# Optimization experiments

Measured on AMD Instinct MI355X. Metric: run time of the kernel, lower is better.

The kernel has to match this reference:

```python
import jax, jax.numpy as jnp
import numpy as np

RADIUS = 0.1
NSAMPLE = 32


def _ball_query(radius, nsample, xyz, new_xyz):
    # xyz: (B,N,3), new_xyz: (B,npoint,3) -> idx (B,npoint,nsample) int32
    # Faithful to the CUDA ball_query: take the first nsample in-radius indices
    # (in ascending point order); pad with the first found index.
    N = xyz.shape[1]
    d2 = jnp.sum((new_xyz[:, :, None, :] - xyz[:, None, :, :]) ** 2, axis=-1)  # (B,np,N)
    mask = d2 < radius * radius
    key_arr = jnp.where(mask, jnp.arange(N, dtype=jnp.int32), jnp.int32(N))
    idx = jnp.sort(key_arr, axis=-1)[..., :nsample]  # (B,np,ns)
    first = idx[..., :1]
    idx = jnp.where(idx == N, first, idx)
    idx = jnp.where(idx == N, 0, idx)  # empty-ball fallback (matches zero-init buffer)
    return idx


def _group(features, idx):
    # features (B,C,N), idx (B,np,ns) -> (B,C,np,ns)
    return jax.vmap(lambda f, i: f[:, i])(features, idx)


def _forward(xyz, new_xyz):
    idx = jax.lax.stop_gradient(_ball_query(RADIUS, NSAMPLE, xyz, new_xyz))
    xyz_t = jnp.transpose(xyz, (0, 2, 1))                 # (B,3,N)
    g = _group(xyz_t, idx)                                # (B,3,np,ns) grouped_xyz
    c = jnp.transpose(new_xyz, (0, 2, 1))[..., None]      # (B,3,np,1)  new_xyz_reshaped

    # pairwise distances within each group
    diff = g[..., :, None] - g[..., None, :]              # (B,3,np,ns,ns)
    dis = jnp.sqrt(jnp.sum(diff * diff, axis=1))          # (B,np,ns,ns)
    mean_dis = jnp.mean(dis, axis=3)                      # (B,np,ns)
    tip_idx = jnp.argmax(mean_dis, axis=2)                # (B,np)
    tip_pts = jnp.take_along_axis(g, tip_idx[:, None, :, None], axis=3)[..., 0]  # (B,3,np)

    cb = jnp.broadcast_to(c, g.shape)                     # (B,3,np,ns)
    gpv = jnp.cross(jnp.cross(cb, g, axis=1), cb, axis=1)
    gpv = gpv / jnp.linalg.norm(gpv, axis=1)[:, None]     # (B,3,np,ns)

    new_r = jnp.sqrt(jnp.sum(c * c, axis=1))              # (B,np,1)
    new_norm = c / (new_r[:, None] + 1e-8)                # (B,3,np,1)

    c3 = c[..., 0]                                        # (B,3,np)
    tpv = jnp.cross(jnp.cross(c3, tip_pts, axis=1), c3, axis=1)
    tpv = tpv / jnp.linalg.norm(tpv, axis=1)[:, None]     # (B,3,np)

    gcv = jnp.cross(gpv, jnp.broadcast_to(tpv[..., None], gpv.shape), axis=1)
    sinv = jnp.sum(gcv * new_norm, axis=1)                # (B,np,ns)

    dis_t = jnp.transpose(dis, (0, 2, 1, 3))              # (B,ns,np,ns)
    dis_sort = jnp.sort(dis_t, axis=1) * sinv[:, None]    # (B,ns,np,ns)
    grouped_r = jnp.sqrt(jnp.sum(g * g, axis=1))          # (B,np,ns)
    return jnp.concatenate([dis_sort, grouped_r[:, None]], axis=1)  # (B,ns+1,np,ns)


def setup_inputs() -> dict:
    key = jax.random.key(0)
    k1, k2 = jax.random.split(key)
    xyz = jax.random.uniform(k1, (4, 16384, 3), dtype=jnp.float32)
    new_xyz = jax.random.uniform(k2, (4, 2048, 3), dtype=jnp.float32)
    return {"xyz": xyz, "new_xyz": new_xyz}


def reference(xyz, new_xyz):
    return _forward(xyz, new_xyz)
```

## Files before the change

### kernel.cpp

```cpp
#include <hip/hip_runtime.h>


#define BB 4
#define NN 16384
#define MM 2048
#define NS 32
#define R2 0.01f
#define NCELL 1000
#define CPAD 1024
#define HCAP 128

#define WS_PTS_OFF (16 * 1024)
#define WS_NEED (WS_PTS_OFF + (size_t)BB * NN * 16)

__device__ __forceinline__ int cell_of(float x, float y, float z) {
    int ci = (int)(x * 10.0f); ci = ci < 0 ? 0 : (ci > 9 ? 9 : ci);
    int cj = (int)(y * 10.0f); cj = cj < 0 ? 0 : (cj > 9 ? 9 : cj);
    int ck = (int)(z * 10.0f); ck = ck < 0 ? 0 : (ck > 9 ? 9 : ck);
    return (ci * 10 + cj) * 10 + ck;
}

__global__ __launch_bounds__(1024) void k_build(const float* __restrict__ xyz,
                                                int* __restrict__ off,
                                                float4* __restrict__ pts) {
    __shared__ int sc[1024];
    __shared__ int sa[1024];
    const int b = blockIdx.x, t = threadIdx.x;
    sc[t] = 0;
    __syncthreads();
    const float* xp = xyz + (size_t)b * NN * 3;
    float X[16], Y[16], Z[16]; int C[16];
    #pragma unroll
    for (int k = 0; k < 16; ++k) {
        int i = k * 1024 + t;
        const float* p = xp + (size_t)i * 3;
        X[k] = p[0]; Y[k] = p[1]; Z[k] = p[2];
        C[k] = cell_of(X[k], Y[k], Z[k]);
        atomicAdd(&sc[C[k]], 1);
    }
    __syncthreads();
    int v = sc[t];
    sa[t] = v;
    __syncthreads();
    for (int s = 1; s < 1024; s <<= 1) {
        int u = (t >= s) ? sa[t - s] : 0;
        __syncthreads();
        sa[t] += u;
        __syncthreads();
    }
    int excl = sa[t] - v;
    if (t < NCELL) off[b * CPAD + t] = excl;
    if (t == NCELL - 1) off[b * CPAD + NCELL] = sa[t];
    __syncthreads();
    sc[t] = excl;
    __syncthreads();
    #pragma unroll
    for (int k = 0; k < 16; ++k) {
        int pos = atomicAdd(&sc[C[k]], 1);
        int i = k * 1024 + t;
        pts[(size_t)b * NN + pos] = make_float4(X[k], Y[k], Z[k], __int_as_float(i));
    }
}

__global__ __launch_bounds__(256) void qgr_grid_kernel(
    const float* __restrict__ xyz,
    const float* __restrict__ nxyz,
    const int* __restrict__ offi,
    const float4* __restrict__ pts,
    float* __restrict__ out) {

    __shared__ float s_hx[4][HCAP], s_hy[4][HCAP], s_hz[4][HCAP];
    __shared__ int   s_hidx[4][HCAP];

    const int lane = threadIdx.x & 63;
    const int w = threadIdx.x >> 6;
    const int q = blockIdx.x * 4 + w;
    const int b = q >> 11;
    const int m = q & (MM - 1);

    const float* xb = xyz + (size_t)b * NN * 3;
    const float* nq = nxyz + (size_t)q * 3;
    const float cx = nq[0], cy = nq[1], cz = nq[2];
    const unsigned long long lmask = (1ull << lane) - 1ull;

    const int* offb = offi + b * CPAD;
    const float4* ptsb = pts + (size_t)b * NN;

    int ci0 = (int)(cx * 10.0f); ci0 = ci0 < 0 ? 0 : (ci0 > 9 ? 9 : ci0);
    int cj0 = (int)(cy * 10.0f); cj0 = cj0 < 0 ? 0 : (cj0 > 9 ? 9 : cj0);
    int ck0 = (int)(cz * 10.0f); ck0 = ck0 < 0 ? 0 : (ck0 > 9 ? 9 : ck0);
    int zlo = ck0 > 0 ? ck0 - 1 : 0;
    int zhi = ck0 < 9 ? ck0 + 1 : 9;

    int rs[9], rl[9];
    #pragma unroll
    for (int r = 0; r < 9; ++r) { rs[r] = 0; rl[r] = 0; }
    int nr = 0;
    #pragma unroll
    for (int di = -1; di <= 1; ++di) {
        int ii = ci0 + di; if ((unsigned)ii > 9u) continue;
        #pragma unroll
        for (int dj = -1; dj <= 1; ++dj) {
            int jj = cj0 + dj; if ((unsigned)jj > 9u) continue;
            int base2 = (ii * 10 + jj) * 10;
            int s0 = offb[base2 + zlo];
            int e0 = offb[base2 + zhi + 1];
            int len = e0 - s0;
            if (len > 0) { rs[nr] = s0; rl[nr] = len; ++nr; }
        }
    }

    float4 P[9];
    #pragma unroll
    for (int r = 0; r < 9; ++r) {
        int a = (lane < rl[r]) ? (rs[r] + lane) : 0;
        P[r] = ptsb[a];
    }

    int hits = 0;
    #pragma unroll
    for (int r = 0; r < 9; ++r) {
        float dx = __fsub_rn(cx, P[r].x);
        float dy = __fsub_rn(cy, P[r].y);
        float dz = __fsub_rn(cz, P[r].z);
        float d2 = __fadd_rn(__fadd_rn(__fmul_rn(dx, dx), __fmul_rn(dy, dy)),
                             __fmul_rn(dz, dz));
        bool hit = (lane < rl[r]) && (d2 < R2);
        unsigned long long bal = __ballot(hit);
        if (bal) {
            int rank = __popcll(bal & lmask);
            int slot = hits + rank;
            if (hit && slot < HCAP) {
                s_hx[w][slot] = P[r].x; s_hy[w][slot] = P[r].y;
                s_hz[w][slot] = P[r].z; s_hidx[w][slot] = __float_as_int(P[r].w);
            }
            hits += __popcll(bal);
        }
    }
    for (int r = 0; r < nr; ++r) {
        for (int t0 = 64; t0 < rl[r]; t0 += 64) {
            int t = t0 + lane;
            bool act = t < rl[r];
            float4 Q = ptsb[rs[r] + (act ? t : 0)];
            float dx = __fsub_rn(cx, Q.x);
            float dy = __fsub_rn(cy, Q.y);
            float dz = __fsub_rn(cz, Q.z);
            float d2 = __fadd_rn(__fadd_rn(__fmul_rn(dx, dx), __fmul_rn(dy, dy)),
                                 __fmul_rn(dz, dz));
            bool hit = act && (d2 < R2);
            unsigned long long bal = __ballot(hit);
            if (bal) {
                int rank = __popcll(bal & lmask);
                int slot = hits + rank;
                if (hit && slot < HCAP) {
                    s_hx[w][slot] = Q.x; s_hy[w][slot] = Q.y;
                    s_hz[w][slot] = Q.z; s_hidx[w][slot] = __float_as_int(Q.w);
                }
                hits += __popcll(bal);
            }
        }
    }

    int cap = hits < HCAP ? hits : HCAP;
    int key0 = (lane < cap)      ? ((s_hidx[w][lane] << 8) | lane)            : 0x7fffffff;
    int key1 = (64 + lane < cap) ? ((s_hidx[w][64 + lane] << 8) | (64 + lane)) : 0x7fffffff;

    #pragma unroll
    for (int k = 2; k <= 128; k <<= 1) {
        #pragma unroll
        for (int j = k >> 1; j > 0; j >>= 1) {
            if (j >= 64) {
                int lo = min(key0, key1), hi = max(key0, key1);
                key0 = lo; key1 = hi;
            } else {
                int p0 = __shfl_xor(key0, j);
                int p1 = __shfl_xor(key1, j);
                bool lower = (lane & j) == 0;
                bool up0, up1;
                if (k >= 128)     { up0 = true;             up1 = true; }
                else if (k == 64) { up0 = true;             up1 = false; }
                else              { up0 = (lane & k) == 0;  up1 = up0; }
                key0 = (lower == up0) ? min(key0, p0) : max(key0, p0);
                key1 = (lower == up1) ? min(key1, p1) : max(key1, p1);
            }
        }
    }

    const int found = hits < NS ? hits : NS;
    const int j = lane & 31;
    int skey = __shfl(key0, j);
    float hx = 0.f, hy = 0.f, hz = 0.f;
    if (j < found) {
        int s = skey & 0xFF;
        hx = s_hx[w][s]; hy = s_hy[w][s]; hz = s_hz[w][s];
    }
    float p0x, p0y, p0z;
    if (found == 0) { p0x = xb[0]; p0y = xb[1]; p0z = xb[2]; }
    else { p0x = __shfl(hx, 0); p0y = __shfl(hy, 0); p0z = __shfl(hz, 0); }
    if (j >= found) { hx = p0x; hy = p0y; hz = p0z; }

    float v[NS];
    #pragma unroll
    for (int ii = 0; ii < NS; ++ii) {
        float bx = __shfl(hx, ii), by = __shfl(hy, ii), bz = __shfl(hz, ii);
        float dx = __fsub_rn(bx, hx);
        float dy = __fsub_rn(by, hy);
        float dz = __fsub_rn(bz, hz);
        v[ii] = sqrtf(__fadd_rn(__fadd_rn(__fmul_rn(dx, dx), __fmul_rn(dy, dy)),
                                __fmul_rn(dz, dz)));
    }

    float r8[8];
    #pragma unroll
    for (int t = 0; t < 8; ++t) {
        r8[t] = __fadd_rn(__fadd_rn(__fadd_rn(v[t], v[t + 8]), v[t + 16]), v[t + 24]);
    }
    float mv = __fadd_rn(__fadd_rn(__fadd_rn(r8[0], r8[1]), __fadd_rn(r8[2], r8[3])),
                         __fadd_rn(__fadd_rn(r8[4], r8[5]), __fadd_rn(r8[6], r8[7])));
    int mi = j;
    #pragma unroll
    for (int off = 1; off < 64; off <<= 1) {
        float ov = __shfl_xor(mv, off);
        int oi = __shfl_xor(mi, off);
        if (ov > mv || (ov == mv && oi < mi)) { mv = ov; mi = oi; }
    }

    float tx = __shfl(hx, mi), ty = __shfl(hy, mi), tz = __shfl(hz, mi);

    float ux = cy * tz - cz * ty, uy = cz * tx - cx * tz, uz = cx * ty - cy * tx;
    float vx = uy * cz - uz * cy, vy = uz * cx - ux * cz, vz = ux * cy - uy * cx;
    float vn = fmaxf(sqrtf(vx * vx + vy * vy + vz * vz), 1e-37f);
    float tnx = vx / vn, tny = vy / vn, tnz = vz / vn;

    float nrm = sqrtf(cx * cx + cy * cy + cz * cz);
    float dn = nrm + 1e-8f;
    float nnx = cx / dn, nny = cy / dn, nnz = cz / dn;

    float ax = cy * hz - cz * hy, ay = cz * hx - cx * hz, az = cx * hy - cy * hx;
    float px = ay * cz - az * cy, py = az * cx - ax * cz, pz = ax * cy - ay * cx;
    float pn = fmaxf(sqrtf(px * px + py * py + pz * pz), 1e-37f);
    px /= pn; py /= pn; pz /= pn;

    float qx = py * tnz - pz * tny;
    float qy = pz * tnx - px * tnz;
    float qz = px * tny - py * tnx;
    float sinv = qx * nnx + qy * nny + qz * nnz;

    float gr = sqrtf(hx * hx + hy * hy + hz * hz);

    const size_t rowstride = (size_t)MM * NS;
    const size_t obase = (((size_t)b * 33) * MM + m) * NS + j;
    if (lane < NS) out[obase + 32 * rowstride] = gr;

    #pragma unroll
    for (int k = 2; k <= NS; k <<= 1) {
        #pragma unroll
        for (int jj = k >> 1; jj > 0; jj >>= 1) {
            #pragma unroll
            for (int ii = 0; ii < NS; ++ii) {
                int ll = ii ^ jj;
                if (ll > ii) {
                    bool up = ((ii & k) == 0);
                    float a = v[ii], c2 = v[ll];
                    bool sw = up ? (a > c2) : (a < c2);
                    if (sw) { v[ii] = c2; v[ll] = a; }
                }
            }
        }
    }

    if (lane < NS) {
        #pragma unroll
        for (int ii = 0; ii < NS; ++ii)
            out[obase + (size_t)ii * rowstride] = v[ii] * sinv;
    }
}

#define CHUNKS 4
__global__ __launch_bounds__(256) void qgr_kernel(
    const float* __restrict__ xyz,
    const float* __restrict__ nxyz,
    float* __restrict__ out) {

    __shared__ float s_gx[4][NS], s_gy[4][NS], s_gz[4][NS];
    __shared__ float s_dis[4][NS][NS + 1];

    const int lane = threadIdx.x & 63;
    const int w = threadIdx.x >> 6;
    const int q = blockIdx.x * 4 + w;
    const int b = q >> 11;
    const int m = q & (MM - 1);

    const float* xb = xyz + (size_t)b * NN * 3;
    const float* nq = nxyz + (size_t)q * 3;
    const float cx = nq[0], cy = nq[1], cz = nq[2];
    const unsigned long long lmask = (1ull << lane) - 1ull;

    int cnt = 0;
    for (int base = 0; base < NN; base += 64 * CHUNKS) {
        float X[CHUNKS], Y[CHUNKS], Z[CHUNKS];
        #pragma unroll
        for (int c = 0; c < CHUNKS; ++c) {
            const float* p = xb + (size_t)(base + c * 64 + lane) * 3;
            X[c] = p[0]; Y[c] = p[1]; Z[c] = p[2];
        }
        bool in[CHUNKS];
        #pragma unroll
        for (int c = 0; c < CHUNKS; ++c) {
            float dx = __fsub_rn(cx, X[c]);
            float dy = __fsub_rn(cy, Y[c]);
            float dz = __fsub_rn(cz, Z[c]);
            float d2 = __fadd_rn(__fadd_rn(__fmul_rn(dx, dx), __fmul_rn(dy, dy)),
                                 __fmul_rn(dz, dz));
            in[c] = d2 < R2;
        }
        #pragma unroll
        for (int c = 0; c < CHUNKS; ++c) {
            unsigned long long bal = __ballot(in[c]);
            if (bal) {
                int rank = __popcll(bal & lmask);
                int slot = cnt + rank;
                if (in[c] && slot < NS) {
                    s_gx[w][slot] = X[c]; s_gy[w][slot] = Y[c]; s_gz[w][slot] = Z[c];
                }
                cnt += __popcll(bal);
            }
        }
        if (cnt >= NS) break;
    }
    __syncthreads();

    int found = cnt < NS ? cnt : NS;
    float p0x, p0y, p0z;
    if (found == 0) { p0x = xb[0]; p0y = xb[1]; p0z = xb[2]; }
    else            { p0x = s_gx[w][0]; p0y = s_gy[w][0]; p0z = s_gz[w][0]; }
    if (lane < NS && lane >= found) {
        s_gx[w][lane] = p0x; s_gy[w][lane] = p0y; s_gz[w][lane] = p0z;
    }
    __syncthreads();

    #pragma unroll
    for (int t = 0; t < 16; ++t) {
        int e = t * 64 + lane;
        int di = e >> 5, dj = e & 31;
        float dx = __fsub_rn(s_gx[w][di], s_gx[w][dj]);
        float dy = __fsub_rn(s_gy[w][di], s_gy[w][dj]);
        float dz = __fsub_rn(s_gz[w][di], s_gz[w][dj]);
        s_dis[w][di][dj] =
            sqrtf(__fadd_rn(__fadd_rn(__fmul_rn(dx, dx), __fmul_rn(dy, dy)), __fmul_rn(dz, dz)));
    }
    __syncthreads();

    {
        int i = lane & 31;
        float r[8];
        #pragma unroll
        for (int t = 0; t < 8; ++t) {
            r[t] = __fadd_rn(__fadd_rn(__fadd_rn(s_dis[w][i][t], s_dis[w][i][t + 8]),
                                        s_dis[w][i][t + 16]),
                             s_dis[w][i][t + 24]);
        }
        float mv = __fadd_rn(__fadd_rn(__fadd_rn(r[0], r[1]), __fadd_rn(r[2], r[3])),
                             __fadd_rn(__fadd_rn(r[4], r[5]), __fadd_rn(r[6], r[7])));
        int mi = i;
        #pragma unroll
        for (int off = 1; off < 64; off <<= 1) {
            float ov = __shfl_xor(mv, off);
            int oi = __shfl_xor(mi, off);
            if (ov > mv || (ov == mv && oi < mi)) { mv = ov; mi = oi; }
        }
        float tx = s_gx[w][mi], ty = s_gy[w][mi], tz = s_gz[w][mi];
        float ux = cy * tz - cz * ty, uy = cz * tx - cx * tz, uz = cx * ty - cy * tx;
        float vx = uy * cz - uz * cy, vy = uz * cx - ux * cz, vz = ux * cy - uy * cx;
        float vn = fmaxf(sqrtf(vx * vx + vy * vy + vz * vz), 1e-37f);
        float tnx = vx / vn, tny = vy / vn, tnz = vz / vn;
        float nr = sqrtf(cx * cx + cy * cy + cz * cz);
        float dn = nr + 1e-8f;
        float nnx = cx / dn, nny = cy / dn, nnz = cz / dn;
        int j = lane & 31;
        float gx = s_gx[w][j], gy = s_gy[w][j], gz = s_gz[w][j];
        float ax = cy * gz - cz * gy, ay = cz * gx - cx * gz, az = cx * gy - cy * gx;
        float px = ay * cz - az * cy, py = az * cx - ax * cz, pz = ax * cy - ay * cx;
        float pn = fmaxf(sqrtf(px * px + py * py + pz * pz), 1e-37f);
        px /= pn; py /= pn; pz /= pn;
        float qx = py * tnz - pz * tny;
        float qy = pz * tnx - px * tnz;
        float qz = px * tny - py * tnx;
        float sinv = qx * nnx + qy * nny + qz * nnz;
        float gr = sqrtf(gx * gx + gy * gy + gz * gz);
        const size_t rowstride = (size_t)MM * NS;
        const size_t obase = (((size_t)b * 33) * MM + m) * NS + j;
        if (lane < NS) out[obase + 32 * rowstride] = gr;
        float v[NS];
        #pragma unroll
        for (int ii = 0; ii < NS; ++ii) v[ii] = s_dis[w][ii][j];
        #pragma unroll
        for (int k = 2; k <= NS; k <<= 1) {
            #pragma unroll
            for (int jj = k >> 1; jj > 0; jj >>= 1) {
                #pragma unroll
                for (int ii = 0; ii < NS; ++ii) {
                    int ll = ii ^ jj;
                    if (ll > ii) {
                        bool up = ((ii & k) == 0);
                        float a = v[ii], c2 = v[ll];
                        bool sw = up ? (a > c2) : (a < c2);
                        if (sw) { v[ii] = c2; v[ll] = a; }
                    }
                }
            }
        }
        if (lane < NS) {
            #pragma unroll
            for (int ii = 0; ii < NS; ++ii)
                out[obase + (size_t)ii * rowstride] = v[ii] * sinv;
        }
    }
}

extern "C" void kernel_launch(void* const* d_in, const int* in_sizes, int n_in,
                              void* d_out, int out_size, void* d_ws, size_t ws_size,
                              hipStream_t stream) {
    (void)in_sizes; (void)n_in; (void)out_size;
    const float* xyz = (const float*)d_in[0];
    const float* nxyz = (const float*)d_in[1];
    float* out = (float*)d_out;

    if (d_ws != nullptr && ws_size >= WS_NEED) {
        char* ws = (char*)d_ws;
        int* off = (int*)ws;
        float4* pts = (float4*)(ws + WS_PTS_OFF);
        k_build<<<BB, 1024, 0, stream>>>(xyz, off, pts);
        qgr_grid_kernel<<<(BB * MM) / 4, 256, 0, stream>>>(xyz, nxyz, off, pts, out);
    } else {
        qgr_kernel<<<(BB * MM) / 4, 256, 0, stream>>>(xyz, nxyz, out);
    }
}
```

Baseline: 114.8 us.

## Process two queries per wavefront and use shuffle-based scan in grid build

The grid query kernel now has each 64-lane wavefront handle two query points. The neighbor search runs sequentially for both, and each 32-lane half then runs the sort, pairwise-distance and output stages for its own query, so all lanes do useful work in the per-group compute instead of half idling. The hit-index sort becomes a 32-lane bitonic sort over four registers per lane. The build kernel replaces the shared-memory Hillis-Steele prefix scan, which needed many barriers, with a wave shuffle scan plus per-wave sums. In exchange, the two neighbor searches run back to back, which lengthens that phase per wave, and the launch uses half as many blocks.

New measurement: 105.3 us. 8.2% less time.

```diff
diff --git a/kernel.cpp b/kernel.cpp
--- a/kernel.cpp
+++ b/kernel.cpp
@@ -24,8 +24,9 @@
                                                 int* __restrict__ off,
                                                 float4* __restrict__ pts) {
     __shared__ int sc[1024];
-    __shared__ int sa[1024];
+    __shared__ int wsum[16];
     const int b = blockIdx.x, t = threadIdx.x;
+    const int lane = t & 63, wid = t >> 6;
     sc[t] = 0;
     __syncthreads();
     const float* xp = xyz + (size_t)b * NN * 3;
@@ -40,17 +41,21 @@
     }
     __syncthreads();
     int v = sc[t];
-    sa[t] = v;
-    __syncthreads();
-    for (int s = 1; s < 1024; s <<= 1) {
-        int u = (t >= s) ? sa[t - s] : 0;
-        __syncthreads();
-        sa[t] += u;
-        __syncthreads();
-    }
-    int excl = sa[t] - v;
+    int x = v;
+    #pragma unroll
+    for (int o = 1; o < 64; o <<= 1) {
+        int u = __shfl_up(x, o);
+        if (lane >= o) x += u;
+    }
+    if (lane == 63) wsum[wid] = x;
+    __syncthreads();
+    int pre = 0;
+    #pragma unroll
+    for (int i2 = 0; i2 < 16; ++i2) pre += (i2 < wid) ? wsum[i2] : 0;
+    int incl = x + pre;
+    int excl = incl - v;
     if (t < NCELL) off[b * CPAD + t] = excl;
-    if (t == NCELL - 1) off[b * CPAD + NCELL] = sa[t];
+    if (t == 1023) off[b * CPAD + NCELL] = incl;
     __syncthreads();
     sc[t] = excl;
     __syncthreads();
@@ -69,140 +74,193 @@
     const float4* __restrict__ pts,
     float* __restrict__ out) {
 
-    __shared__ float s_hx[4][HCAP], s_hy[4][HCAP], s_hz[4][HCAP];
-    __shared__ int   s_hidx[4][HCAP];
+    __shared__ float s_hx[4][2][HCAP], s_hy[4][2][HCAP], s_hz[4][2][HCAP];
+    __shared__ int   s_hidx[4][2][HCAP];
 
     const int lane = threadIdx.x & 63;
     const int w = threadIdx.x >> 6;
-    const int q = blockIdx.x * 4 + w;
-    const int b = q >> 11;
-    const int m = q & (MM - 1);
+    const int sub = lane & 31;
+    const int half = lane >> 5;
+    const int q0 = blockIdx.x * 8 + w * 2;
+    const int b = q0 >> 11;
 
     const float* xb = xyz + (size_t)b * NN * 3;
-    const float* nq = nxyz + (size_t)q * 3;
-    const float cx = nq[0], cy = nq[1], cz = nq[2];
+    const float* nq = nxyz + (size_t)q0 * 3;
+    const float cx0 = nq[0], cy0 = nq[1], cz0 = nq[2];
+    const float cx1 = nq[3], cy1 = nq[4], cz1 = nq[5];
     const unsigned long long lmask = (1ull << lane) - 1ull;
 
     const int* offb = offi + b * CPAD;
     const float4* ptsb = pts + (size_t)b * NN;
 
-    int ci0 = (int)(cx * 10.0f); ci0 = ci0 < 0 ? 0 : (ci0 > 9 ? 9 : ci0);
-    int cj0 = (int)(cy * 10.0f); cj0 = cj0 < 0 ? 0 : (cj0 > 9 ? 9 : cj0);
-    int ck0 = (int)(cz * 10.0f); ck0 = ck0 < 0 ? 0 : (ck0 > 9 ? 9 : ck0);
-    int zlo = ck0 > 0 ? ck0 - 1 : 0;
-    int zhi = ck0 < 9 ? ck0 + 1 : 9;
-
-    int rs[9], rl[9];
-    #pragma unroll
-    for (int r = 0; r < 9; ++r) { rs[r] = 0; rl[r] = 0; }
-    int nr = 0;
-    #pragma unroll
-    for (int di = -1; di <= 1; ++di) {
-        int ii = ci0 + di; if ((unsigned)ii > 9u) continue;
-        #pragma unroll
-        for (int dj = -1; dj <= 1; ++dj) {
-            int jj = cj0 + dj; if ((unsigned)jj > 9u) continue;
-            int base2 = (ii * 10 + jj) * 10;
-            int s0 = offb[base2 + zlo];
-            int e0 = offb[base2 + zhi + 1];
-            int len = e0 - s0;
-            if (len > 0) { rs[nr] = s0; rl[nr] = len; ++nr; }
-        }
-    }
-
-    float4 P[9];
-    #pragma unroll
-    for (int r = 0; r < 9; ++r) {
-        int a = (lane < rl[r]) ? (rs[r] + lane) : 0;
-        P[r] = ptsb[a];
-    }
-
-    int hits = 0;
-    #pragma unroll
-    for (int r = 0; r < 9; ++r) {
-        float dx = __fsub_rn(cx, P[r].x);
-        float dy = __fsub_rn(cy, P[r].y);
-        float dz = __fsub_rn(cz, P[r].z);
-        float d2 = __fadd_rn(__fadd_rn(__fmul_rn(dx, dx), __fmul_rn(dy, dy)),
-                             __fmul_rn(dz, dz));
-        bool hit = (lane < rl[r]) && (d2 < R2);
-        unsigned long long bal = __ballot(hit);
-        if (bal) {
-            int rank = __popcll(bal & lmask);
-            int slot = hits + rank;
-            if (hit && slot < HCAP) {
-                s_hx[w][slot] = P[r].x; s_hy[w][slot] = P[r].y;
-                s_hz[w][slot] = P[r].z; s_hidx[w][slot] = __float_as_int(P[r].w);
-            }
-            hits += __popcll(bal);
-        }
-    }
-    for (int r = 0; r < nr; ++r) {
-        for (int t0 = 64; t0 < rl[r]; t0 += 64) {
-            int t = t0 + lane;
-            bool act = t < rl[r];
-            float4 Q = ptsb[rs[r] + (act ? t : 0)];
-            float dx = __fsub_rn(cx, Q.x);
-            float dy = __fsub_rn(cy, Q.y);
-            float dz = __fsub_rn(cz, Q.z);
+    int hits01[2];
+    for (int tq = 0; tq < 2; ++tq) {
+        const float ccx = tq ? cx1 : cx0;
+        const float ccy = tq ? cy1 : cy0;
+        const float ccz = tq ? cz1 : cz0;
+
+        int ci0 = (int)(ccx * 10.0f); ci0 = ci0 < 0 ? 0 : (ci0 > 9 ? 9 : ci0);
+        int cj0 = (int)(ccy * 10.0f); cj0 = cj0 < 0 ? 0 : (cj0 > 9 ? 9 : cj0);
+        int ck0 = (int)(ccz * 10.0f); ck0 = ck0 < 0 ? 0 : (ck0 > 9 ? 9 : ck0);
+        int zlo = ck0 > 0 ? ck0 - 1 : 0;
+        int zhi = ck0 < 9 ? ck0 + 1 : 9;
+
+        int rs[9], rl[9];
+        #pragma unroll
+        for (int r = 0; r < 9; ++r) { rs[r] = 0; rl[r] = 0; }
+        int nr = 0;
+        #pragma unroll
+        for (int di = -1; di <= 1; ++di) {
+            int ii = ci0 + di; if ((unsigned)ii > 9u) continue;
+            #pragma unroll
+            for (int dj = -1; dj <= 1; ++dj) {
+                int jj = cj0 + dj; if ((unsigned)jj > 9u) continue;
+                int base2 = (ii * 10 + jj) * 10;
+                int s0 = offb[base2 + zlo];
+                int e0 = offb[base2 + zhi + 1];
+                int len = e0 - s0;
+                if (len > 0) { rs[nr] = s0; rl[nr] = len; ++nr; }
+            }
+        }
+
+        float4 P[9];
+        #pragma unroll
+        for (int r = 0; r < 9; ++r) {
+            int a = (lane < rl[r]) ? (rs[r] + lane) : 0;
+            P[r] = ptsb[a];
+        }
+
+        int hits = 0;
+        #pragma unroll
+        for (int r = 0; r < 9; ++r) {
+            float dx = __fsub_rn(ccx, P[r].x);
+            float dy = __fsub_rn(ccy, P[r].y);
+            float dz = __fsub_rn(ccz, P[r].z);
             float d2 = __fadd_rn(__fadd_rn(__fmul_rn(dx, dx), __fmul_rn(dy, dy)),
                                  __fmul_rn(dz, dz));
-            bool hit = act && (d2 < R2);
+            bool hit = (lane < rl[r]) && (d2 < R2);
             unsigned long long bal = __ballot(hit);
             if (bal) {
                 int rank = __popcll(bal & lmask);
                 int slot = hits + rank;
                 if (hit && slot < HCAP) {
-                    s_hx[w][slot] = Q.x; s_hy[w][slot] = Q.y;
-                    s_hz[w][slot] = Q.z; s_hidx[w][slot] = __float_as_int(Q.w);
+                    s_hx[w][tq][slot] = P[r].x; s_hy[w][tq][slot] = P[r].y;
+                    s_hz[w][tq][slot] = P[r].z; s_hidx[w][tq][slot] = __float_as_int(P[r].w);
                 }
                 hits += __popcll(bal);
             }
         }
-    }
-
-    int cap = hits < HCAP ? hits : HCAP;
-    int key0 = (lane < cap)      ? ((s_hidx[w][lane] << 8) | lane)            : 0x7fffffff;
-    int key1 = (64 + lane < cap) ? ((s_hidx[w][64 + lane] << 8) | (64 + lane)) : 0x7fffffff;
-
-    #pragma unroll
-    for (int k = 2; k <= 128; k <<= 1) {
+        for (int r = 0; r < nr; ++r) {
+            for (int t0 = 64; t0 < rl[r]; t0 += 64) {
+                int t = t0 + lane;
+                bool act = t < rl[r];
+                float4 Q = ptsb[rs[r] + (act ? t : 0)];
+                float dx = __fsub_rn(ccx, Q.x);
+                float dy = __fsub_rn(ccy, Q.y);
+                float dz = __fsub_rn(ccz, Q.z);
+                float d2 = __fadd_rn(__fadd_rn(__fmul_rn(dx, dx), __fmul_rn(dy, dy)),
+                                     __fmul_rn(dz, dz));
+                bool hit = act && (d2 < R2);
+                unsigned long long bal = __ballot(hit);
+                if (bal) {
+                    int rank = __popcll(bal & lmask);
+                    int slot = hits + rank;
+                    if (hit && slot < HCAP) {
+                        s_hx[w][tq][slot] = Q.x; s_hy[w][tq][slot] = Q.y;
+                        s_hz[w][tq][slot] = Q.z; s_hidx[w][tq][slot] = __float_as_int(Q.w);
+                    }
+                    hits += __popcll(bal);
+                }
+            }
+        }
+        hits01[tq] = hits;
+    }
+
+    const int hits = half ? hits01[1] : hits01[0];
+    const int cap = hits < HCAP ? hits : HCAP;
+    const float ccx = half ? cx1 : cx0;
+    const float ccy = half ? cy1 : cy0;
+    const float ccz = half ? cz1 : cz0;
+
+    int key[4];
+    #pragma unroll
+    for (int r = 0; r < 4; ++r) {
+        int e = r * 32 + sub;
+        key[r] = (e < cap) ? ((s_hidx[w][half][e] << 8) | e) : 0x7fffffff;
+    }
+
+    #pragma unroll
+    for (int k = 2; k <= 16; k <<= 1) {
         #pragma unroll
         for (int j = k >> 1; j > 0; j >>= 1) {
-            if (j >= 64) {
-                int lo = min(key0, key1), hi = max(key0, key1);
-                key0 = lo; key1 = hi;
-            } else {
-                int p0 = __shfl_xor(key0, j);
-                int p1 = __shfl_xor(key1, j);
-                bool lower = (lane & j) == 0;
-                bool up0, up1;
-                if (k >= 128)     { up0 = true;             up1 = true; }
-                else if (k == 64) { up0 = true;             up1 = false; }
-                else              { up0 = (lane & k) == 0;  up1 = up0; }
-                key0 = (lower == up0) ? min(key0, p0) : max(key0, p0);
-                key1 = (lower == up1) ? min(key1, p1) : max(key1, p1);
-            }
+            bool lower = (sub & j) == 0;
+            bool asc = (sub & k) == 0;
+            bool keepmin = (lower == asc);
+            #pragma unroll
+            for (int r = 0; r < 4; ++r) {
+                int p = __shfl_xor(key[r], j);
+                key[r] = keepmin ? min(key[r], p) : max(key[r], p);
+            }
+        }
+    }
+    #pragma unroll
+    for (int j = 16; j > 0; j >>= 1) {
+        bool lower = (sub & j) == 0;
+        #pragma unroll
+        for (int r = 0; r < 4; ++r) {
+            int p = __shfl_xor(key[r], j);
+            bool asc = (r & 1) == 0;
+            key[r] = (lower == asc) ? min(key[r], p) : max(key[r], p);
+        }
+    }
+    {
+        int t0 = min(key[0], key[1]); key[1] = max(key[0], key[1]); key[0] = t0;
+        int t2 = max(key[2], key[3]); key[3] = min(key[2], key[3]); key[2] = t2;
+    }
+    #pragma unroll
+    for (int j = 16; j > 0; j >>= 1) {
+        bool lower = (sub & j) == 0;
+        #pragma unroll
+        for (int r = 0; r < 4; ++r) {
+            int p = __shfl_xor(key[r], j);
+            bool asc = (r & 2) == 0;
+            key[r] = (lower == asc) ? min(key[r], p) : max(key[r], p);
+        }
+    }
+    {
+        int t0 = min(key[0], key[2]); key[2] = max(key[0], key[2]); key[0] = t0;
+        int t1 = min(key[1], key[3]); key[3] = max(key[1], key[3]); key[1] = t1;
+        t0 = min(key[0], key[1]); key[1] = max(key[0], key[1]); key[0] = t0;
+        t1 = min(key[2], key[3]); key[3] = max(key[2], key[3]); key[2] = t1;
+    }
+    #pragma unroll
+    for (int j = 16; j > 0; j >>= 1) {
+        bool lower = (sub & j) == 0;
+        #pragma unroll
+        for (int r = 0; r < 4; ++r) {
+            int p = __shfl_xor(key[r], j);
+            key[r] = lower ? min(key[r], p) : max(key[r], p);
         }
     }
 
     const int found = hits < NS ? hits : NS;
-    const int j = lane & 31;
-    int skey = __shfl(key0, j);
+    const int hbase = half << 5;
     float hx = 0.f, hy = 0.f, hz = 0.f;
-    if (j < found) {
-        int s = skey & 0xFF;
-        hx = s_hx[w][s]; hy = s_hy[w][s]; hz = s_hz[w][s];
+    if (sub < found) {
+        int s = key[0] & 0xFF;
+        hx = s_hx[w][half][s]; hy = s_hy[w][half][s]; hz = s_hz[w][half][s];
     }
     float p0x, p0y, p0z;
     if (found == 0) { p0x = xb[0]; p0y = xb[1]; p0z = xb[2]; }
-    else { p0x = __shfl(hx, 0); p0y = __shfl(hy, 0); p0z = __shfl(hz, 0); }
-    if (j >= found) { hx = p0x; hy = p0y; hz = p0z; }
+    else { p0x = __shfl(hx, hbase); p0y = __shfl(hy, hbase); p0z = __shfl(hz, hbase); }
+    if (sub >= found) { hx = p0x; hy = p0y; hz = p0z; }
 
     float v[NS];
     #pragma unroll
     for (int ii = 0; ii < NS; ++ii) {
-        float bx = __shfl(hx, ii), by = __shfl(hy, ii), bz = __shfl(hz, ii);
+        float bx = __shfl(hx, hbase + ii);
+        float by = __shfl(hy, hbase + ii);
+        float bz = __shfl(hz, hbase + ii);
         float dx = __fsub_rn(bx, hx);
         float dy = __fsub_rn(by, hy);
         float dz = __fsub_rn(bz, hz);
@@ -217,27 +275,27 @@
     }
     float mv = __fadd_rn(__fadd_rn(__fadd_rn(r8[0], r8[1]), __fadd_rn(r8[2], r8[3])),
                          __fadd_rn(__fadd_rn(r8[4], r8[5]), __fadd_rn(r8[6], r8[7])));
-    int mi = j;
-    #pragma unroll
-    for (int off = 1; off < 64; off <<= 1) {
+    int mi = sub;
+    #pragma unroll
+    for (int off = 1; off < 32; off <<= 1) {
         float ov = __shfl_xor(mv, off);
         int oi = __shfl_xor(mi, off);
         if (ov > mv || (ov == mv && oi < mi)) { mv = ov; mi = oi; }
     }
 
-    float tx = __shfl(hx, mi), ty = __shfl(hy, mi), tz = __shfl(hz, mi);
-
-    float ux = cy * tz - cz * ty, uy = cz * tx - cx * tz, uz = cx * ty - cy * tx;
-    float vx = uy * cz - uz * cy, vy = uz * cx - ux * cz, vz = ux * cy - uy * cx;
+    float tx = __shfl(hx, hbase + mi), ty = __shfl(hy, hbase + mi), tz = __shfl(hz, hbase + mi);
+
+    float ux = ccy * tz - ccz * ty, uy = ccz * tx - ccx * tz, uz = ccx * ty - ccy * tx;
+    float vx = uy * ccz - uz * ccy, vy = uz * ccx - ux * ccz, vz = ux * ccy - uy * ccx;
     float vn = fmaxf(sqrtf(vx * vx + vy * vy + vz * vz), 1e-37f);
     float tnx = vx / vn, tny = vy / vn, tnz = vz / vn;
 
-    float nrm = sqrtf(cx * cx + cy * cy + cz * cz);
+    float nrm = sqrtf(ccx * ccx + ccy * ccy + ccz * ccz);
     float dn = nrm + 1e-8f;
-    float nnx = cx / dn, nny = cy / dn, nnz = cz / dn;
-
-    float ax = cy * hz - cz * hy, ay = cz * hx - cx * hz, az = cx * hy - cy * hx;
-    float px = ay * cz - az * cy, py = az * cx - ax * cz, pz = ax * cy - ay * cx;
+    float nnx = ccx / dn, nny = ccy / dn, nnz = ccz / dn;
+
+    float ax = ccy * hz - ccz * hy, ay = ccz * hx - ccx * hz, az = ccx * hy - ccy * hx;
+    float px = ay * ccz - az * ccy, py = az * ccx - ax * ccz, pz = ax * ccy - ay * ccx;
     float pn = fmaxf(sqrtf(px * px + py * py + pz * pz), 1e-37f);
     px /= pn; py /= pn; pz /= pn;
 
@@ -248,9 +306,10 @@
 
     float gr = sqrtf(hx * hx + hy * hy + hz * hz);
 
+    const int m_h = (q0 + half) & (MM - 1);
     const size_t rowstride = (size_t)MM * NS;
-    const size_t obase = (((size_t)b * 33) * MM + m) * NS + j;
-    if (lane < NS) out[obase + 32 * rowstride] = gr;
+    const size_t obase = (((size_t)b * 33) * MM + m_h) * NS + sub;
+    out[obase + 32 * rowstride] = gr;
 
     #pragma unroll
     for (int k = 2; k <= NS; k <<= 1) {
@@ -269,11 +328,9 @@
         }
     }
 
-    if (lane < NS) {
-        #pragma unroll
-        for (int ii = 0; ii < NS; ++ii)
-            out[obase + (size_t)ii * rowstride] = v[ii] * sinv;
-    }
+    #pragma unroll
+    for (int ii = 0; ii < NS; ++ii)
+        out[obase + (size_t)ii * rowstride] = v[ii] * sinv;
 }
 
 #define CHUNKS 4
@@ -431,7 +488,7 @@
         int* off = (int*)ws;
         float4* pts = (float4*)(ws + WS_PTS_OFF);
         k_build<<<BB, 1024, 0, stream>>>(xyz, off, pts);
-        qgr_grid_kernel<<<(BB * MM) / 4, 256, 0, stream>>>(xyz, nxyz, off, pts, out);
+        qgr_grid_kernel<<<(BB * MM) / 8, 256, 0, stream>>>(xyz, nxyz, off, pts, out);
     } else {
         qgr_kernel<<<(BB * MM) / 4, 256, 0, stream>>>(xyz, nxyz, out);
     }
```
